# Kernel optimization log

Hardware: AMD Instinct MI355X
Metric: run time of the kernel (lower is better)

The kernel has to match this reference:

```python
import jax, jax.numpy as jnp
import numpy as np

NEG_SLOPE = 0.2  # PyG GATConv default negative_slope
N_GRAPHS = 128


def gat_conv(x, src, dst, w, a_src, a_dst, b):
    """PyG GATConv (v1), concat=True. x:[N,F], src/dst:[E] (self-loops included),
    w:[F,H*C], a_src/a_dst:[H,C], b:[H*C]."""
    N = x.shape[0]
    H, C = a_src.shape
    h = (x @ w).reshape(N, H, C)                      # [N,H,C]
    e = (h * a_src).sum(-1)[src] + (h * a_dst).sum(-1)[dst]  # [E,H]
    e = jnp.where(e > 0, e, NEG_SLOPE * e)            # leaky_relu
    m = jax.ops.segment_max(e, dst, num_segments=N)   # per-dst softmax max
    ex = jnp.exp(e - m[dst])
    s = jax.ops.segment_sum(ex, dst, num_segments=N)
    alpha = ex / (s[dst] + 1e-16)                     # [E,H]
    out = jax.ops.segment_sum(h[src] * alpha[:, :, None], dst, num_segments=N)
    return out.reshape(N, H * C) + b


def pool(x, batch, num_graphs):
    """concat(global_mean_pool, global_max_pool)."""
    ones = jnp.ones((x.shape[0],), x.dtype)
    cnt = jax.ops.segment_sum(ones, batch, num_segments=num_graphs)
    mean = jax.ops.segment_sum(x, batch, num_segments=num_graphs) / jnp.maximum(cnt, 1.0)[:, None]
    mx = jax.ops.segment_max(x, batch, num_segments=num_graphs)
    return jnp.concatenate([mean, mx], axis=-1)


def setup_inputs() -> dict:
    key = jax.random.key(0)
    ks = jax.random.split(key, 30)
    N, E, G = 100000, 800000, N_GRAPHS
    F_in, H, C = 260, 4, 64
    HC = H * C  # 256

    def lin(k, i, o):
        return (jax.random.normal(k, (i, o), jnp.float32) * (1.0 / np.sqrt(i)))

    def att(k):
        return jax.random.normal(k, (H, C), jnp.float32) * 0.1

    return {
        "x": jax.random.normal(ks[0], (N, F_in), jnp.float32),
        "edge_index": jax.random.randint(ks[1], (2, E), 0, N),
        "batch": jnp.sort(jax.random.randint(ks[2], (N,), 0, G)),
        "gat1_w": lin(ks[3], F_in, HC), "gat1_as": att(ks[4]), "gat1_ad": att(ks[5]),
        "gat1_b": jnp.zeros((HC,), jnp.float32),
        "lin1_w": lin(ks[6], HC, C), "lin1_b": jnp.zeros((C,), jnp.float32),
        "gat2_w": lin(ks[7], C, HC), "gat2_as": att(ks[8]), "gat2_ad": att(ks[9]),
        "gat2_b": jnp.zeros((HC,), jnp.float32),
        "lin2_w": lin(ks[10], HC, C), "lin2_b": jnp.zeros((C,), jnp.float32),
        "sum_w": lin(ks[11], 4 * C, 2 * C), "sum_b": jnp.zeros((2 * C,), jnp.float32),
        "sh1_w": lin(ks[12], 2 * C, C), "sh1_b": jnp.zeros((C,), jnp.float32),
        "sh2_w": lin(ks[13], C, C), "sh2_b": jnp.zeros((C,), jnp.float32),
        "sh3_w": lin(ks[14], C, C), "sh3_b": jnp.zeros((C,), jnp.float32),
        "reg_w": lin(ks[15], C, 32), "reg_b": jnp.zeros((32,), jnp.float32),
    }


def reference(x, edge_index, batch,
              gat1_w, gat1_as, gat1_ad, gat1_b, lin1_w, lin1_b,
              gat2_w, gat2_as, gat2_ad, gat2_b, lin2_w, lin2_b,
              sum_w, sum_b, sh1_w, sh1_b, sh2_w, sh2_b, sh3_w, sh3_b,
              reg_w, reg_b):
    N = x.shape[0]
    loop = jnp.arange(N)
    src = jnp.concatenate([edge_index[0], loop])  # add_self_loops=True
    dst = jnp.concatenate([edge_index[1], loop])

    h = gat_conv(x, src, dst, gat1_w, gat1_as, gat1_ad, gat1_b)
    h = jax.nn.selu(h @ lin1_w + lin1_b)
    x1 = pool(h, batch, N_GRAPHS)                 # [G, 2C]

    h = gat_conv(h, src, dst, gat2_w, gat2_as, gat2_ad, gat2_b)
    h = jax.nn.selu(h @ lin2_w + lin2_b)
    x2 = pool(h, batch, N_GRAPHS)                 # [G, 2C]

    z = jnp.concatenate([x1, x2], axis=-1) @ sum_w + sum_b
    z = jax.nn.selu(z @ sh1_w + sh1_b)
    z = jax.nn.selu(z @ sh2_w + sh2_b)
    z = jax.nn.selu(z @ sh3_w + sh3_b)
    return z @ reg_w + reg_b                      # [G, 32]
```

## Files before the change

### kernel.cpp

```cpp
#include <hip/hip_runtime.h>
#include <hip/hip_bf16.h>
#include <cstdint>

#define NEG_SLOPE 0.2f
#define HEADS 4
#define CH 64
#define HC 256
#define F_IN 260
#define KPAD1 288
#define NGRAPH 128

typedef __attribute__((ext_vector_type(8))) short bf16x8;
typedef __attribute__((ext_vector_type(8))) unsigned short u16x8;
typedef __attribute__((ext_vector_type(4))) float f32x4;

__device__ __forceinline__ float seluf(float x){
    const float sc=1.0507009873554805f, al=1.6732632423543772f;
    return x>0.f ? sc*x : sc*al*(__expf(x)-1.f);
}
__device__ __forceinline__ unsigned fenc(float x){
    unsigned u=__float_as_uint(x);
    return (u&0x80000000u)? ~u : (u|0x80000000u);
}
__device__ __forceinline__ float fdec(unsigned e){
    unsigned u = (e&0x80000000u)? (e&0x7fffffffu) : ~e;
    return __uint_as_float(u);
}
__device__ __forceinline__ float bf2f(unsigned short u){
    return __uint_as_float(((unsigned)u)<<16);
}
__device__ __forceinline__ unsigned short f2bf_raw(float x){
    unsigned u = __float_as_uint(x);
    unsigned rounded = u + 0x7fffu + ((u >> 16) & 1u);
    return (unsigned short)(rounded >> 16);
}
__device__ __forceinline__ void gload_lds16(const void* g, void* l){
    __builtin_amdgcn_global_load_lds(
        (const __attribute__((address_space(1))) void*)g,
        (__attribute__((address_space(3))) void*)l, 16, 0, 0);
}

__global__ void fill_u32_kernel(unsigned* p, unsigned v, int n){
    int i = blockIdx.x*blockDim.x + threadIdx.x;
    for (; i<n; i += gridDim.x*blockDim.x) p[i]=v;
}

__global__ void degree_kernel(const int* __restrict__ ei, int* __restrict__ deg, int E){
    int i = blockIdx.x*blockDim.x+threadIdx.x;
    for (; i<E; i+=gridDim.x*blockDim.x) atomicAdd(&deg[ei[E+i]], 1);
}

__global__ void scan_ph1(const int* __restrict__ deg, int* __restrict__ bsum, int N){
    __shared__ int sd[256];
    int base = blockIdx.x*1024;
    int t = threadIdx.x;
    int tot=0;
    for(int u=0;u<4;u++){ int i = base + t*4+u; tot += (i<N)? deg[i]:0; }
    sd[t]=tot; __syncthreads();
    for(int off=128; off; off>>=1){ if(t<off) sd[t]+=sd[t+off]; __syncthreads(); }
    if(t==0) bsum[blockIdx.x]=sd[0];
}
__global__ void scan_ph2(int* bsum, int nb, int* rowptr, int N, int E){
    if(threadIdx.x==0 && blockIdx.x==0){
        int run=0;
        for(int b=0;b<nb;b++){ int v=bsum[b]; bsum[b]=run; run+=v; }
        rowptr[N]=E;
    }
}
__global__ void scan_ph3(const int* __restrict__ deg, const int* __restrict__ bsum,
                         int* __restrict__ rowptr, int N){
    __shared__ int sd[256];
    int base = blockIdx.x*1024;
    int t = threadIdx.x;
    int v[4]; int tot=0;
    for(int u=0;u<4;u++){ int i=base+t*4+u; v[u] = (i<N)? deg[i]:0; tot+=v[u]; }
    sd[t]=tot; __syncthreads();
    for(int off=1; off<256; off<<=1){
        int add = (t>=off)? sd[t-off] : 0;
        __syncthreads();
        sd[t] += add;
        __syncthreads();
    }
    int pre = bsum[blockIdx.x] + ((t==0)?0: sd[t-1]);
    for(int u=0;u<4;u++){ int i=base+t*4+u; if(i<N){ rowptr[i]=pre; pre+=v[u]; } }
}

__global__ void scatter_kernel(const int* __restrict__ ei, const int* __restrict__ rowptr,
                               int* __restrict__ fil, int* __restrict__ col, int E){
    int i = blockIdx.x*blockDim.x+threadIdx.x;
    for(; i<E; i+=gridDim.x*blockDim.x){
        int s = ei[i], d = ei[E+i];
        int p = atomicAdd(&fil[d],1);
        col[rowptr[d]+p] = s;
    }
}

__global__ void cvt_x_kernel(const float* __restrict__ x, unsigned* __restrict__ xb, int N){
    int i = blockIdx.x*blockDim.x+threadIdx.x;
    int total = N*(KPAD1/2);
    for (; i<total; i+=gridDim.x*blockDim.x){
        int row = i/(KPAD1/2);
        int c2 = (i - row*(KPAD1/2))*2;
        float v0 = (c2   < F_IN) ? x[(size_t)row*F_IN + c2]   : 0.f;
        float v1 = (c2+1 < F_IN) ? x[(size_t)row*F_IN + c2+1] : 0.f;
        xb[i] = ((unsigned)f2bf_raw(v1) << 16) | f2bf_raw(v0);
    }
}

__global__ void cvt_wT_kernel(const float* __restrict__ w, __hip_bfloat16* __restrict__ wt,
                              int K, int NC, int Kpad){
    int i = blockIdx.x*blockDim.x+threadIdx.x;
    if (i >= NC*Kpad) return;
    int n = i / Kpad, k = i - n*Kpad;
    wt[i] = __float2bfloat16(k < K ? w[(size_t)k*NC + n] : 0.f);
}

template<int BN, int FS>
__global__ __launch_bounds__(512, 4) void mfma_gemm_kernel(
    const __hip_bfloat16* __restrict__ A, int Kpad,
    const __hip_bfloat16* __restrict__ Bt,
    const float* __restrict__ bias, int act,
    __hip_bfloat16* __restrict__ Cb,
    const float* __restrict__ asrc, const float* __restrict__ adst,
    float* __restrict__ ss, float* __restrict__ sdv,
    int M, int NC)
{
    constexpr int NF = BN/32;
    constexpr int WN = BN/2;
    constexpr int TP = WN + 8;
    __shared__ __align__(16) char lds[32768];

    int tid  = threadIdx.x;
    int lane = tid & 63;
    int w    = tid >> 6;
    int wr = w >> 1, wc = w & 1;
    int row0 = blockIdx.x * 128;
    int col0 = blockIdx.y * BN;
    int fr   = lane & 15;
    int koff = (lane >> 4) * 16;

    f32x4 acc[2][NF];
    #pragma unroll
    for (int i=0;i<2;i++)
        #pragma unroll
        for (int j=0;j<NF;j++) acc[i][j] = (f32x4){0.f,0.f,0.f,0.f};

    int lrow = lane >> 2;
    int lcolB = (lane & 3) * 16;
    int ktiles = Kpad >> 5;

    auto stage = [&](int kt, int pb){
        int k0b = kt*64;
        char* Asb = lds + pb*8192;
        char* Bsb = lds + 16384 + pb*(BN*64);
        {
            int gr = row0 + w*16 + lrow; if (gr > M-1) gr = M-1;
            gload_lds16((const char*)A + (size_t)gr*Kpad*2 + k0b + lcolB,
                        Asb + w*1024 + lrow*64 + lcolB);
        }
        if (w < BN/16){
            int gn = col0 + w*16 + lrow;
            gload_lds16((const char*)Bt + (size_t)gn*Kpad*2 + k0b + lcolB,
                        Bsb + w*1024 + lrow*64 + lcolB);
        }
    };

    stage(0, 0);
    __syncthreads();
    for (int kt=0; kt<ktiles; kt++){
        int pb = kt & 1;
        if (kt+1 < ktiles) stage(kt+1, pb^1);
        const char* Ab = lds + pb*8192;
        const char* Bb = lds + 16384 + pb*(BN*64);
        bf16x8 a[2], b[NF];
        a[0] = *(const bf16x8*)(Ab + (wr*32 +      fr)*64 + koff);
        a[1] = *(const bf16x8*)(Ab + (wr*32 + 16 + fr)*64 + koff);
        #pragma unroll
        for (int nt=0; nt<NF; nt++)
            b[nt] = *(const bf16x8*)(Bb + (wc*WN + nt*16 + fr)*64 + koff);
        #pragma unroll
        for (int mt=0; mt<2; mt++)
            #pragma unroll
            for (int nt=0; nt<NF; nt++)
                acc[mt][nt] = __builtin_amdgcn_mfma_f32_16x16x32_bf16(a[mt], b[nt], acc[mt][nt], 0, 0, 0);
        __syncthreads();
    }

    if (FS){
        float asv[NF], adv[NF];
        #pragma unroll
        for (int nt=0; nt<NF; nt++){
            int gc = col0 + wc*WN + nt*16 + fr;
            asv[nt] = asrc[gc];
            adv[nt] = adst[gc];
        }
        int head = (col0 + wc*WN) >> 6;
        #pragma unroll
        for (int mt=0; mt<2; mt++){
            #pragma unroll
            for (int r=0; r<4; r++){
                float ts=0.f, td=0.f;
                #pragma unroll
                for (int nt=0; nt<NF; nt++){
                    ts = fmaf(acc[mt][nt][r], asv[nt], ts);
                    td = fmaf(acc[mt][nt][r], adv[nt], td);
                }
                #pragma unroll
                for (int off=1; off<16; off<<=1){
                    ts += __shfl_xor(ts, off);
                    td += __shfl_xor(td, off);
                }
                if (fr==0){
                    int gr = row0 + wr*32 + mt*16 + (lane>>4)*4 + r;
                    if (gr < M){ ss[gr*4+head]=ts; sdv[gr*4+head]=td; }
                }
            }
        }
    }

    char* ct = lds + w*(16*TP*2);
    int c0 = col0 + wc*WN;
    #pragma unroll
    for (int mt=0; mt<2; mt++){
        #pragma unroll
        for (int nt=0; nt<NF; nt++){
            #pragma unroll
            for (int r=0; r<4; r++){
                float v = acc[mt][nt][r];
                if (bias) v += bias[c0 + nt*16 + fr];
                if (act)  v = seluf(v);
                int tr = (lane>>4)*4 + r;
                *(unsigned short*)(ct + tr*(TP*2) + (nt*16+fr)*2) = f2bf_raw(v);
            }
        }
        constexpr int CPR = WN/8;
        constexpr int RPP = 64/CPR;
        #pragma unroll
        for (int p=0; p<16/RPP; p++){
            int tr = p*RPP + lane/CPR;
            int ch = lane % CPR;
            int4 v = *(const int4*)(ct + tr*(TP*2) + ch*16);
            int gr = row0 + wr*32 + mt*16 + tr;
            if (gr < M)
                *(int4*)((char*)Cb + ((size_t)gr*NC + c0 + ch*8)*2) = v;
        }
    }
}

__global__ void softmax_prep_kernel(const float* __restrict__ ss, const float* __restrict__ sdv,
                                    const int* __restrict__ rowptr, const int* __restrict__ col,
                                    float2* __restrict__ minv, float* __restrict__ selfa, int N){
    int t = blockIdx.x*blockDim.x + threadIdx.x;
    int node = t >> 2;
    int h = t & 3;
    if (node >= N) return;
    float ad = sdv[node*4+h];
    float e0 = ss[node*4+h] + ad;
    e0 = e0>0.f ? e0 : NEG_SLOPE*e0;
    float m = e0, s = 1.f;
    int jb = rowptr[node], je = rowptr[node+1];
    for (int j=jb; j<je; j++){
        int sc = col[j];
        float e = ss[sc*4+h] + ad;
        e = e>0.f ? e : NEG_SLOPE*e;
        float mn = fmaxf(m, e);
        s = s*__expf(m-mn) + __expf(e-mn);
        m = mn;
    }
    float inv = 1.f / s;
    minv[node*4+h] = make_float2(m, inv);
    selfa[node*4+h] = __expf(e0-m)*inv;
}

__global__ void aggregate2_kernel(const __hip_bfloat16* __restrict__ h,
                                  const float* __restrict__ ss, const float* __restrict__ sdv,
                                  const float2* __restrict__ minv, const float* __restrict__ selfa,
                                  const int* __restrict__ rowptr, const int* __restrict__ col,
                                  const float* __restrict__ bias,
                                  __hip_bfloat16* __restrict__ outp, int N){
    int node = blockIdx.x*4 + (threadIdx.x>>6);
    if (node >= N) return;
    int lane = threadIdx.x & 63;
    int s = lane >> 4;
    int t = lane & 15;
    int hh = t >> 2;
    const unsigned short* hp = (const unsigned short*)h;

    float ad = sdv[node*4+hh];
    float2 mi = minv[node*4+hh];

    float acc[16];
    {
        float sa = (s==0) ? selfa[node*4+hh] : 0.f;
        const unsigned short* base = hp + (size_t)node*HC + t*16;
        u16x8 v0 = *(const u16x8*)(base);
        u16x8 v1 = *(const u16x8*)(base + 8);
        #pragma unroll
        for (int k=0;k<8;k++){
            acc[k]   = sa * bf2f(v0[k]);
            acc[8+k] = sa * bf2f(v1[k]);
        }
    }

    int jb = rowptr[node], je = rowptr[node+1];
    for (int j0 = jb; j0 < je; j0 += 8){
        int jA = j0 + s;
        int jB = j0 + s + 4;
        int scA = (jA < je) ? col[jA] : node;
        int scB = (jB < je) ? col[jB] : node;
        const unsigned short* bA = hp + (size_t)scA*HC + t*16;
        const unsigned short* bB = hp + (size_t)scB*HC + t*16;
        u16x8 a0 = *(const u16x8*)bA;
        u16x8 a1 = *(const u16x8*)(bA + 8);
        u16x8 b0 = *(const u16x8*)bB;
        u16x8 b1 = *(const u16x8*)(bB + 8);
        float eA = ss[scA*4+hh] + ad;
        float eB = ss[scB*4+hh] + ad;
        eA = eA>0.f ? eA : NEG_SLOPE*eA;
        eB = eB>0.f ? eB : NEG_SLOPE*eB;
        float pA = (jA < je) ? __expf(eA - mi.x)*mi.y : 0.f;
        float pB = (jB < je) ? __expf(eB - mi.x)*mi.y : 0.f;
        #pragma unroll
        for (int k=0;k<8;k++){
            acc[k]   = fmaf(pA, bf2f(a0[k]), acc[k]);
            acc[8+k] = fmaf(pA, bf2f(a1[k]), acc[8+k]);
        }
        #pragma unroll
        for (int k=0;k<8;k++){
            acc[k]   = fmaf(pB, bf2f(b0[k]), acc[k]);
            acc[8+k] = fmaf(pB, bf2f(b1[k]), acc[8+k]);
        }
    }

    #pragma unroll
    for (int k=0;k<16;k++){
        acc[k] += __shfl_xor(acc[k], 16);
        acc[k] += __shfl_xor(acc[k], 32);
    }

    if (s==0){
        unsigned d[8];
        #pragma unroll
        for (int k=0;k<8;k++){
            unsigned lo = f2bf_raw(acc[2*k]   + bias[t*16 + 2*k]);
            unsigned hi = f2bf_raw(acc[2*k+1] + bias[t*16 + 2*k+1]);
            d[k] = lo | (hi<<16);
        }
        unsigned short* op = (unsigned short*)outp + (size_t)node*HC + t*16;
        int4 w0 = make_int4((int)d[0], (int)d[1], (int)d[2], (int)d[3]);
        int4 w1 = make_int4((int)d[4], (int)d[5], (int)d[6], (int)d[7]);
        *(int4*)op = w0;
        *(int4*)(op + 8) = w1;
    }
}

__global__ void count_kernel(const int* __restrict__ batch, int* __restrict__ cnt, int N){
    int i = blockIdx.x*blockDim.x + threadIdx.x;
    if (i >= N) return;
    int lane = threadIdx.x & 63;
    int g = batch[i];
    int nfull = N & ~63;
    if (i < nfull){
        int g0 = __shfl(g, 0);
        if (__all(g==g0)){ if (lane==0) atomicAdd(&cnt[g0], 64); }
        else atomicAdd(&cnt[g], 1);
    } else {
        atomicAdd(&cnt[g], 1);
    }
}

__global__ void pool_kernel(const __hip_bfloat16* __restrict__ hs, const int* __restrict__ batch,
                            float* __restrict__ psum, unsigned* __restrict__ pmax, int N){
    int c = threadIdx.x & 63;
    int sub = threadIdx.x >> 6;
    int n0 = blockIdx.x*128 + sub*32;
    const unsigned short* hp = (const unsigned short*)hs;
    float s = 0.f, mx = -__builtin_inff();
    int cur = -1;
    for (int j=0; j<32; j++){
        int n = n0 + j;
        if (n >= N) break;
        int g = batch[n];
        if (g != cur){
            if (cur >= 0){
                atomicAdd(&psum[cur*64+c], s);
                atomicMax(&pmax[cur*64+c], fenc(mx));
            }
            cur = g; s = 0.f; mx = -__builtin_inff();
        }
        float v = bf2f(hp[(size_t)n*64 + c]);
        s += v; mx = fmaxf(mx, v);
    }
    if (cur >= 0){
        atomicAdd(&psum[cur*64+c], s);
        atomicMax(&pmax[cur*64+c], fenc(mx));
    }
}

__global__ void pool_final_kernel(const float* __restrict__ psum, const unsigned* __restrict__ pmax,
                                  const int* __restrict__ cnt, float* __restrict__ x, int G){
    int i = blockIdx.x*blockDim.x+threadIdx.x;
    if (i >= G*64) return;
    int g=i>>6, c=i&63;
    float cf = fmaxf((float)cnt[g], 1.f);
    x[g*128 + c] = psum[i]/cf;
    x[g*128 + 64 + c] = fdec(pmax[i]);
}

__global__ __launch_bounds__(128) void head_kernel(
    const float* __restrict__ x1, const float* __restrict__ x2,
    const float* __restrict__ sw, const float* __restrict__ sb,
    const float* __restrict__ w1, const float* __restrict__ b1,
    const float* __restrict__ w2, const float* __restrict__ b2,
    const float* __restrict__ w3, const float* __restrict__ b3,
    const float* __restrict__ rw, const float* __restrict__ rb,
    float* __restrict__ out)
{
    int g = blockIdx.x, t = threadIdx.x;
    __shared__ float v[256], z1[128], z2[64], z3[64], z4[64];
    v[t] = x1[g*128+t];
    v[128+t] = x2[g*128+t];
    __syncthreads();
    float a = sb[t];
    for(int k=0;k<256;k++) a = fmaf(v[k], sw[k*128+t], a);
    z1[t] = a;
    __syncthreads();
    if(t<64){
        float a2 = b1[t];
        for(int k=0;k<128;k++) a2 = fmaf(z1[k], w1[k*64+t], a2);
        z2[t] = seluf(a2);
    }
    __syncthreads();
    if(t<64){
        float a3 = b2[t];
        for(int k=0;k<64;k++) a3 = fmaf(z2[k], w2[k*64+t], a3);
        z3[t] = seluf(a3);
    }
    __syncthreads();
    if(t<64){
        float a4 = b3[t];
        for(int k=0;k<64;k++) a4 = fmaf(z3[k], w3[k*64+t], a4);
        z4[t] = seluf(a4);
    }
    __syncthreads();
    if(t<32){
        float a5 = rb[t];
        for(int k=0;k<64;k++) a5 = fmaf(z4[k], rw[k*32+t], a5);
        out[g*32+t] = a5;
    }
}

extern "C" void kernel_launch(void* const* d_in, const int* in_sizes, int n_in,
                              void* d_out, int out_size, void* d_ws, size_t ws_size,
                              hipStream_t stream)
{
    const float* x    = (const float*)d_in[0];
    const int*   ei   = (const int*)d_in[1];
    const int*   batch= (const int*)d_in[2];
    const float* g1w  = (const float*)d_in[3];
    const float* g1as = (const float*)d_in[4];
    const float* g1ad = (const float*)d_in[5];
    const float* g1b  = (const float*)d_in[6];
    const float* l1w  = (const float*)d_in[7];
    const float* l1b  = (const float*)d_in[8];
    const float* g2w  = (const float*)d_in[9];
    const float* g2as = (const float*)d_in[10];
    const float* g2ad = (const float*)d_in[11];
    const float* g2b  = (const float*)d_in[12];
    const float* l2w  = (const float*)d_in[13];
    const float* l2b  = (const float*)d_in[14];
    const float* sw   = (const float*)d_in[15];
    const float* sb   = (const float*)d_in[16];
    const float* s1w  = (const float*)d_in[17];
    const float* s1b  = (const float*)d_in[18];
    const float* s2w  = (const float*)d_in[19];
    const float* s2b  = (const float*)d_in[20];
    const float* s3w  = (const float*)d_in[21];
    const float* s3b  = (const float*)d_in[22];
    const float* rw   = (const float*)d_in[23];
    const float* rb   = (const float*)d_in[24];
    float* out = (float*)d_out;

    const int N = in_sizes[0] / F_IN;
    const int E = in_sizes[1] / 2;
    const int G = NGRAPH;

    char* ws = (char*)d_ws;
    size_t off = 0;
    auto alloc = [&](size_t bytes)->void*{
        void* p = ws + off;
        off += (bytes + 255) & ~(size_t)255;
        return p;
    };
    int* deg     = (int*)alloc((size_t)2*N*4);
    int* fil     = deg + N;
    int* rowptr  = (int*)alloc(((size_t)N+1)*4);
    int* col     = (int*)alloc((size_t)E*4);
    int* bsum    = (int*)alloc(1024);
    int* zpool   = (int*)alloc((size_t)(128 + 2*G*64)*4);
    int*   cnt = zpool;
    float* PS1 = (float*)(zpool + 128);
    float* PS2 = PS1 + G*64;
    unsigned* PM1 = (unsigned*)alloc((size_t)2*G*64*4);
    unsigned* PM2 = PM1 + G*64;
    float* X1    = (float*)alloc((size_t)G*128*4);
    float* X2    = (float*)alloc((size_t)G*128*4);
    __hip_bfloat16* Xb  = (__hip_bfloat16*)alloc((size_t)N*KPAD1*2);
    __hip_bfloat16* W1t = (__hip_bfloat16*)alloc((size_t)HC*KPAD1*2);
    __hip_bfloat16* L1t = (__hip_bfloat16*)alloc((size_t)CH*HC*2);
    __hip_bfloat16* W2t = (__hip_bfloat16*)alloc((size_t)HC*CH*2);
    __hip_bfloat16* L2t = (__hip_bfloat16*)alloc((size_t)CH*HC*2);
    __hip_bfloat16* Abf = (__hip_bfloat16*)alloc((size_t)N*HC*2);
    __hip_bfloat16* Bbf = (__hip_bfloat16*)alloc((size_t)N*HC*2);
    __hip_bfloat16* HSb = (__hip_bfloat16*)alloc((size_t)N*CH*2);
    float* SCS   = (float*)alloc((size_t)N*HEADS*4);
    float* SCD   = (float*)alloc((size_t)N*HEADS*4);
    float2* MNV  = (float2*)alloc((size_t)N*HEADS*8);
    float* SELFA = (float*)alloc((size_t)N*HEADS*4);
    (void)ws_size; (void)n_in; (void)out_size;

    const unsigned ENC_NEG_INF = 0x007FFFFFu;
    int nb = (N+1023)/1024;

    fill_u32_kernel<<<256,256,0,stream>>>((unsigned*)deg, 0u, 2*N);
    fill_u32_kernel<<<64,256,0,stream>>>((unsigned*)zpool, 0u, 128 + 2*G*64);
    fill_u32_kernel<<<64,256,0,stream>>>(PM1, ENC_NEG_INF, 2*G*64);

    degree_kernel<<<1024,256,0,stream>>>(ei, deg, E);
    scan_ph1<<<nb,256,0,stream>>>(deg, bsum, N);
    scan_ph2<<<1,64,0,stream>>>(bsum, nb, rowptr, N, E);
    scan_ph3<<<nb,256,0,stream>>>(deg, bsum, rowptr, N);
    scatter_kernel<<<1024,256,0,stream>>>(ei, rowptr, fil, col, E);

    cvt_x_kernel<<<2048,256,0,stream>>>(x, (unsigned*)Xb, N);
    cvt_wT_kernel<<<(HC*KPAD1+255)/256,256,0,stream>>>(g1w, W1t, F_IN, HC, KPAD1);
    cvt_wT_kernel<<<(CH*HC+255)/256,256,0,stream>>>(l1w, L1t, HC, CH, HC);
    cvt_wT_kernel<<<(HC*CH+255)/256,256,0,stream>>>(g2w, W2t, CH, HC, CH);
    cvt_wT_kernel<<<(CH*HC+255)/256,256,0,stream>>>(l2w, L2t, HC, CH, HC);

    int nodeBlocks = (N+3)/4;
    int prepBlocks = (N*4+255)/256;
    dim3 gA((N+127)/128, 2);
    dim3 gL((N+127)/128, 1);

    mfma_gemm_kernel<128,1><<<gA,512,0,stream>>>(Xb, KPAD1, W1t, nullptr, 0, Abf,
                                                 g1as, g1ad, SCS, SCD, N, HC);
    softmax_prep_kernel<<<prepBlocks,256,0,stream>>>(SCS, SCD, rowptr, col, MNV, SELFA, N);
    aggregate2_kernel<<<nodeBlocks,256,0,stream>>>(Abf, SCS, SCD, MNV, SELFA, rowptr, col, g1b, Bbf, N);
    mfma_gemm_kernel<64,0><<<gL,512,0,stream>>>(Bbf, HC, L1t, l1b, 1, HSb,
                                                nullptr, nullptr, nullptr, nullptr, N, CH);
    count_kernel<<<(N+255)/256,256,0,stream>>>(batch, cnt, N);
    pool_kernel<<<(N+127)/128,256,0,stream>>>(HSb, batch, PS1, PM1, N);
    pool_final_kernel<<<(G*64+255)/256,256,0,stream>>>(PS1, PM1, cnt, X1, G);

    mfma_gemm_kernel<128,1><<<gA,512,0,stream>>>(HSb, CH, W2t, nullptr, 0, Abf,
                                                 g2as, g2ad, SCS, SCD, N, HC);
    softmax_prep_kernel<<<prepBlocks,256,0,stream>>>(SCS, SCD, rowptr, col, MNV, SELFA, N);
    aggregate2_kernel<<<nodeBlocks,256,0,stream>>>(Abf, SCS, SCD, MNV, SELFA, rowptr, col, g2b, Bbf, N);
    mfma_gemm_kernel<64,0><<<gL,512,0,stream>>>(Bbf, HC, L2t, l2b, 1, HSb,
                                                nullptr, nullptr, nullptr, nullptr, N, CH);
    pool_kernel<<<(N+127)/128,256,0,stream>>>(HSb, batch, PS2, PM2, N);
    pool_final_kernel<<<(G*64+255)/256,256,0,stream>>>(PS2, PM2, cnt, X2, G);

    head_kernel<<<G,128,0,stream>>>(X1, X2, sw, sb, s1w, s1b, s2w, s2b, s3w, s3b, rw, rb, out);
}
```

Before: 513.7 us.

## Fuse softmax prep into aggregation, fold graph counts into pooling, vectorize x conversion

The aggregation kernel now computes the per-destination online softmax max and sum itself. Each wave runs a first pass over the neighbour scores, with per-lane partial states merged by shuffles, so the separate softmax_prep kernel and its intermediate buffers are gone. The node-count kernel is folded into the first pooling kernel through a template flag. The x to bf16 conversion now uses 8-wide float4 loads and int4 stores. Together these cut kernel launches and memory round trips, at the cost of reading col and the scores twice inside the aggregation kernel.

```diff
diff --git a/kernel.cpp b/kernel.cpp
--- a/kernel.cpp
+++ b/kernel.cpp
@@ -97,13 +97,26 @@
 
 __global__ void cvt_x_kernel(const float* __restrict__ x, unsigned* __restrict__ xb, int N){
     int i = blockIdx.x*blockDim.x+threadIdx.x;
-    int total = N*(KPAD1/2);
+    int total = N*36;
     for (; i<total; i+=gridDim.x*blockDim.x){
-        int row = i/(KPAD1/2);
-        int c2 = (i - row*(KPAD1/2))*2;
-        float v0 = (c2   < F_IN) ? x[(size_t)row*F_IN + c2]   : 0.f;
-        float v1 = (c2+1 < F_IN) ? x[(size_t)row*F_IN + c2+1] : 0.f;
-        xb[i] = ((unsigned)f2bf_raw(v1) << 16) | f2bf_raw(v0);
+        int row = i/36;
+        int c = (i - row*36)*8;
+        const float* src = x + (size_t)row*F_IN + c;
+        float v[8];
+        if (c + 8 <= F_IN){
+            float4 a = *(const float4*)src;
+            float4 b = *(const float4*)(src+4);
+            v[0]=a.x; v[1]=a.y; v[2]=a.z; v[3]=a.w;
+            v[4]=b.x; v[5]=b.y; v[6]=b.z; v[7]=b.w;
+        } else {
+            #pragma unroll
+            for (int k=0;k<8;k++) v[k] = (c+k < F_IN) ? src[k] : 0.f;
+        }
+        unsigned d[4];
+        #pragma unroll
+        for (int k=0;k<4;k++)
+            d[k] = (unsigned)f2bf_raw(v[2*k]) | ((unsigned)f2bf_raw(v[2*k+1])<<16);
+        *(int4*)(xb + (size_t)row*144 + (c>>1)) = make_int4((int)d[0],(int)d[1],(int)d[2],(int)d[3]);
     }
 }
 
@@ -247,37 +260,11 @@
     }
 }
 
-__global__ void softmax_prep_kernel(const float* __restrict__ ss, const float* __restrict__ sdv,
-                                    const int* __restrict__ rowptr, const int* __restrict__ col,
-                                    float2* __restrict__ minv, float* __restrict__ selfa, int N){
-    int t = blockIdx.x*blockDim.x + threadIdx.x;
-    int node = t >> 2;
-    int h = t & 3;
-    if (node >= N) return;
-    float ad = sdv[node*4+h];
-    float e0 = ss[node*4+h] + ad;
-    e0 = e0>0.f ? e0 : NEG_SLOPE*e0;
-    float m = e0, s = 1.f;
-    int jb = rowptr[node], je = rowptr[node+1];
-    for (int j=jb; j<je; j++){
-        int sc = col[j];
-        float e = ss[sc*4+h] + ad;
-        e = e>0.f ? e : NEG_SLOPE*e;
-        float mn = fmaxf(m, e);
-        s = s*__expf(m-mn) + __expf(e-mn);
-        m = mn;
-    }
-    float inv = 1.f / s;
-    minv[node*4+h] = make_float2(m, inv);
-    selfa[node*4+h] = __expf(e0-m)*inv;
-}
-
-__global__ void aggregate2_kernel(const __hip_bfloat16* __restrict__ h,
-                                  const float* __restrict__ ss, const float* __restrict__ sdv,
-                                  const float2* __restrict__ minv, const float* __restrict__ selfa,
-                                  const int* __restrict__ rowptr, const int* __restrict__ col,
-                                  const float* __restrict__ bias,
-                                  __hip_bfloat16* __restrict__ outp, int N){
+__global__ void aggregate_fused_kernel(const __hip_bfloat16* __restrict__ h,
+                                       const float* __restrict__ ss, const float* __restrict__ sdv,
+                                       const int* __restrict__ rowptr, const int* __restrict__ col,
+                                       const float* __restrict__ bias,
+                                       __hip_bfloat16* __restrict__ outp, int N){
     int node = blockIdx.x*4 + (threadIdx.x>>6);
     if (node >= N) return;
     int lane = threadIdx.x & 63;
@@ -287,11 +274,48 @@
     const unsigned short* hp = (const unsigned short*)h;
 
     float ad = sdv[node*4+hh];
-    float2 mi = minv[node*4+hh];
+    float e0 = ss[node*4+hh] + ad;
+    e0 = e0>0.f ? e0 : NEG_SLOPE*e0;
+
+    int jb = rowptr[node], je = rowptr[node+1];
+
+    float mA = (s==0) ? e0 : -1e30f;
+    float sA = (s==0) ? 1.f : 0.f;
+    float mB = -1e30f, sB = 0.f;
+    for (int j0 = jb; j0 < je; j0 += 8){
+        int jA = j0 + s, jB = j0 + s + 4;
+        if (jA < je){
+            int sc = col[jA];
+            float e = ss[sc*4+hh] + ad;
+            e = e>0.f ? e : NEG_SLOPE*e;
+            float mn = fmaxf(mA, e);
+            sA = sA*__expf(mA-mn) + __expf(e-mn);
+            mA = mn;
+        }
+        if (jB < je){
+            int sc = col[jB];
+            float e = ss[sc*4+hh] + ad;
+            e = e>0.f ? e : NEG_SLOPE*e;
+            float mn = fmaxf(mB, e);
+            sB = sB*__expf(mB-mn) + __expf(e-mn);
+            mB = mn;
+        }
+    }
+    float m = fmaxf(mA, mB);
+    float sum = sA*__expf(mA-m) + sB*__expf(mB-m);
+    #pragma unroll
+    for (int off=16; off<=32; off<<=1){
+        float mo = __shfl_xor(m, off);
+        float so = __shfl_xor(sum, off);
+        float mn = fmaxf(m, mo);
+        sum = sum*__expf(m-mn) + so*__expf(mo-mn);
+        m = mn;
+    }
+    float inv = 1.f / sum;
 
     float acc[16];
     {
-        float sa = (s==0) ? selfa[node*4+hh] : 0.f;
+        float sa = (s==0) ? __expf(e0-m)*inv : 0.f;
         const unsigned short* base = hp + (size_t)node*HC + t*16;
         u16x8 v0 = *(const u16x8*)(base);
         u16x8 v1 = *(const u16x8*)(base + 8);
@@ -301,8 +325,6 @@
             acc[8+k] = sa * bf2f(v1[k]);
         }
     }
-
-    int jb = rowptr[node], je = rowptr[node+1];
     for (int j0 = jb; j0 < je; j0 += 8){
         int jA = j0 + s;
         int jB = j0 + s + 4;
@@ -318,8 +340,8 @@
         float eB = ss[scB*4+hh] + ad;
         eA = eA>0.f ? eA : NEG_SLOPE*eA;
         eB = eB>0.f ? eB : NEG_SLOPE*eB;
-        float pA = (jA < je) ? __expf(eA - mi.x)*mi.y : 0.f;
-        float pB = (jB < je) ? __expf(eB - mi.x)*mi.y : 0.f;
+        float pA = (jA < je) ? __expf(eA - m)*inv : 0.f;
+        float pB = (jB < je) ? __expf(eB - m)*inv : 0.f;
         #pragma unroll
         for (int k=0;k<8;k++){
             acc[k]   = fmaf(pA, bf2f(a0[k]), acc[k]);
@@ -354,29 +376,16 @@
     }
 }
 
-__global__ void count_kernel(const int* __restrict__ batch, int* __restrict__ cnt, int N){
-    int i = blockIdx.x*blockDim.x + threadIdx.x;
-    if (i >= N) return;
-    int lane = threadIdx.x & 63;
-    int g = batch[i];
-    int nfull = N & ~63;
-    if (i < nfull){
-        int g0 = __shfl(g, 0);
-        if (__all(g==g0)){ if (lane==0) atomicAdd(&cnt[g0], 64); }
-        else atomicAdd(&cnt[g], 1);
-    } else {
-        atomicAdd(&cnt[g], 1);
-    }
-}
-
+template<int DO_COUNT>
 __global__ void pool_kernel(const __hip_bfloat16* __restrict__ hs, const int* __restrict__ batch,
-                            float* __restrict__ psum, unsigned* __restrict__ pmax, int N){
+                            float* __restrict__ psum, unsigned* __restrict__ pmax,
+                            int* __restrict__ cnt, int N){
     int c = threadIdx.x & 63;
     int sub = threadIdx.x >> 6;
     int n0 = blockIdx.x*128 + sub*32;
     const unsigned short* hp = (const unsigned short*)hs;
     float s = 0.f, mx = -__builtin_inff();
-    int cur = -1;
+    int cur = -1, rl = 0;
     for (int j=0; j<32; j++){
         int n = n0 + j;
         if (n >= N) break;
@@ -385,15 +394,17 @@
             if (cur >= 0){
                 atomicAdd(&psum[cur*64+c], s);
                 atomicMax(&pmax[cur*64+c], fenc(mx));
+                if (DO_COUNT && c==0) atomicAdd(&cnt[cur], rl);
             }
-            cur = g; s = 0.f; mx = -__builtin_inff();
+            cur = g; s = 0.f; mx = -__builtin_inff(); rl = 0;
         }
         float v = bf2f(hp[(size_t)n*64 + c]);
-        s += v; mx = fmaxf(mx, v);
+        s += v; mx = fmaxf(mx, v); rl++;
     }
     if (cur >= 0){
         atomicAdd(&psum[cur*64+c], s);
         atomicMax(&pmax[cur*64+c], fenc(mx));
+        if (DO_COUNT && c==0) atomicAdd(&cnt[cur], rl);
     }
 }
 
@@ -515,8 +526,6 @@
     __hip_bfloat16* HSb = (__hip_bfloat16*)alloc((size_t)N*CH*2);
     float* SCS   = (float*)alloc((size_t)N*HEADS*4);
     float* SCD   = (float*)alloc((size_t)N*HEADS*4);
-    float2* MNV  = (float2*)alloc((size_t)N*HEADS*8);
-    float* SELFA = (float*)alloc((size_t)N*HEADS*4);
     (void)ws_size; (void)n_in; (void)out_size;
 
     const unsigned ENC_NEG_INF = 0x007FFFFFu;
@@ -539,27 +548,23 @@
     cvt_wT_kernel<<<(CH*HC+255)/256,256,0,stream>>>(l2w, L2t, HC, CH, HC);
 
     int nodeBlocks = (N+3)/4;
-    int prepBlocks = (N*4+255)/256;
     dim3 gA((N+127)/128, 2);
     dim3 gL((N+127)/128, 1);
 
     mfma_gemm_kernel<128,1><<<gA,512,0,stream>>>(Xb, KPAD1, W1t, nullptr, 0, Abf,
                                                  g1as, g1ad, SCS, SCD, N, HC);
-    softmax_prep_kernel<<<prepBlocks,256,0,stream>>>(SCS, SCD, rowptr, col, MNV, SELFA, N);
-    aggregate2_kernel<<<nodeBlocks,256,0,stream>>>(Abf, SCS, SCD, MNV, SELFA, rowptr, col, g1b, Bbf, N);
+    aggregate_fused_kernel<<<nodeBlocks,256,0,stream>>>(Abf, SCS, SCD, rowptr, col, g1b, Bbf, N);
     mfma_gemm_kernel<64,0><<<gL,512,0,stream>>>(Bbf, HC, L1t, l1b, 1, HSb,
                                                 nullptr, nullptr, nullptr, nullptr, N, CH);
-    count_kernel<<<(N+255)/256,256,0,stream>>>(batch, cnt, N);
-    pool_kernel<<<(N+127)/128,256,0,stream>>>(HSb, batch, PS1, PM1, N);
+    pool_kernel<1><<<(N+127)/128,256,0,stream>>>(HSb, batch, PS1, PM1, cnt, N);
     pool_final_kernel<<<(G*64+255)/256,256,0,stream>>>(PS1, PM1, cnt, X1, G);
 
     mfma_gemm_kernel<128,1><<<gA,512,0,stream>>>(HSb, CH, W2t, nullptr, 0, Abf,
                                                  g2as, g2ad, SCS, SCD, N, HC);
-    softmax_prep_kernel<<<prepBlocks,256,0,stream>>>(SCS, SCD, rowptr, col, MNV, SELFA, N);
-    aggregate2_kernel<<<nodeBlocks,256,0,stream>>>(Abf, SCS, SCD, MNV, SELFA, rowptr, col, g2b, Bbf, N);
+    aggregate_fused_kernel<<<nodeBlocks,256,0,stream>>>(Abf, SCS, SCD, rowptr, col, g2b, Bbf, N);
     mfma_gemm_kernel<64,0><<<gL,512,0,stream>>>(Bbf, HC, L2t, l2b, 1, HSb,
                                                 nullptr, nullptr, nullptr, nullptr, N, CH);
-    pool_kernel<<<(N+127)/128,256,0,stream>>>(HSb, batch, PS2, PM2, N);
+    pool_kernel<0><<<(N+127)/128,256,0,stream>>>(HSb, batch, PS2, PM2, nullptr, N);
     pool_final_kernel<<<(G*64+255)/256,256,0,stream>>>(PS2, PM2, cnt, X2, G);
 
     head_kernel<<<G,128,0,stream>>>(X1, X2, sw, sb, s1w, s1b, s2w, s2b, s3w, s3b, rw, rb, out);
```

Result: faster. 481.9 us (-6.2%).
